# Performance work log

Hardware: AMD Instinct MI355X
Metric: run time of the kernel (lower is better)

## Reference

```python
import jax, jax.numpy as jnp
import numpy as np

N, E, F_IN, DIM, G = 50000, 800000, 128, 128, 512
NUM_GC_LAYERS = 3
S2S_STEPS = 3


def setup_inputs() -> dict:
    key = jax.random.key(0)
    ks = jax.random.split(key, 17)
    s = 0.05
    rn = lambda k, shape: jax.random.normal(k, shape, jnp.float32) * s
    x = jax.random.normal(ks[0], (N, F_IN), jnp.float32)
    edge_index = jax.random.randint(ks[1], (2, E), 0, N)
    batch = jnp.sort(jax.random.randint(ks[2], (N,), 0, G))
    return dict(
        x=x, edge_index=edge_index, batch=batch,
        lin0_W=rn(ks[3], (DIM, F_IN)), lin0_b=rn(ks[4], (DIM,)),
        gin_W1=rn(ks[5], (DIM, DIM)), gin_b1=rn(ks[6], (DIM,)),
        gin_W2=rn(ks[7], (DIM, DIM)), gin_b2=rn(ks[8], (DIM,)),
        gru_Wih=rn(ks[9], (3 * DIM, DIM)), gru_Whh=rn(ks[10], (3 * DIM, DIM)),
        gru_bih=rn(ks[11], (3 * DIM,)), gru_bhh=rn(ks[12], (3 * DIM,)),
        lstm_Wih=rn(ks[13], (4 * DIM, 2 * DIM)), lstm_Whh=rn(ks[14], (4 * DIM, DIM)),
        lstm_bih=rn(ks[15], (4 * DIM,)), lstm_bhh=rn(ks[16], (4 * DIM,)),
    )


def reference(x, edge_index, batch, lin0_W, lin0_b, gin_W1, gin_b1, gin_W2, gin_b2,
              gru_Wih, gru_Whh, gru_bih, gru_bhh,
              lstm_Wih, lstm_Whh, lstm_bih, lstm_bhh):
    src, dst = edge_index[0], edge_index[1]
    out = jax.nn.relu(x @ lin0_W.T + lin0_b)          # [N, DIM]
    h = out                                            # GRU hidden (seq_len=1, 1 layer)
    for _ in range(NUM_GC_LAYERS):
        # GINConv, eps=0: nn(x + sum_{j in N(i)} x_j); scatter-add over edge list
        aggr = jax.ops.segment_sum(out[src], dst, num_segments=N)
        z = out + aggr
        m = jax.nn.relu(jax.nn.relu(z @ gin_W1.T + gin_b1) @ gin_W2.T + gin_b2)
        # single GRU step (PyTorch gate order: r, z, n)
        gx = m @ gru_Wih.T + gru_bih
        gh = h @ gru_Whh.T + gru_bhh
        gxr, gxz, gxn = jnp.split(gx, 3, axis=-1)
        ghr, ghz, ghn = jnp.split(gh, 3, axis=-1)
        r = jax.nn.sigmoid(gxr + ghr)
        zt = jax.nn.sigmoid(gxz + ghz)
        n = jnp.tanh(gxn + r * ghn)
        h = (1.0 - zt) * n + zt * h
        out = h
    # Set2Set pooling (processing_steps=3), LSTM(2*DIM -> DIM), gate order i,f,g,o
    q_star = jnp.zeros((G, 2 * DIM), x.dtype)
    hl = jnp.zeros((G, DIM), x.dtype)
    cl = jnp.zeros((G, DIM), x.dtype)
    for _ in range(S2S_STEPS):
        gates = q_star @ lstm_Wih.T + lstm_bih + hl @ lstm_Whh.T + lstm_bhh
        i, f, g, o = jnp.split(gates, 4, axis=-1)
        cl = jax.nn.sigmoid(f) * cl + jax.nn.sigmoid(i) * jnp.tanh(g)
        hl = jax.nn.sigmoid(o) * jnp.tanh(cl)
        q = hl                                          # [G, DIM]
        e = jnp.sum(out * q[batch], axis=-1)            # [N] attention logits
        emax = jax.lax.stop_gradient(jax.ops.segment_max(e, batch, num_segments=G))
        emax = jnp.where(jnp.isfinite(emax), emax, 0.0)
        a_num = jnp.exp(e - emax[batch])
        denom = jax.ops.segment_sum(a_num, batch, num_segments=G)
        a = a_num / (denom[batch] + 1e-16)              # per-graph softmax
        rvec = jax.ops.segment_sum(a[:, None] * out, batch, num_segments=G)
        q_star = jnp.concatenate([q, rvec], axis=-1)    # [G, 2*DIM]
    return (q_star, out)
```

## Files before the change

kernel.cpp:

```cpp
#include <hip/hip_runtime.h>
#include <hip/hip_bf16.h>
#include <math.h>

static constexpr int NN  = 50000;
static constexpr int NE  = 800000;
static constexpr int DIM = 128;
static constexpr int NG  = 512;
static constexpr int NBLK = (NN + 255) / 256;

typedef __attribute__((ext_vector_type(8))) short bf16x8;
typedef __attribute__((ext_vector_type(4))) float f32x4;
typedef __attribute__((ext_vector_type(8))) float f32x8;

__device__ __forceinline__ float sigm(float x) {
    return __builtin_amdgcn_rcpf(1.0f + __expf(-x));
}
__device__ __forceinline__ float ftanh(float x) {
    x = fminf(fmaxf(x, -15.f), 15.f);
    float t = __expf(2.f * x);
    return (t - 1.f) * __builtin_amdgcn_rcpf(t + 1.f);
}
__device__ __forceinline__ float b2f(ushort u) { return __uint_as_float(((unsigned)u) << 16); }
__device__ __forceinline__ ushort f2b(float f) {
    __hip_bfloat16 h = __float2bfloat16(f);
    return *reinterpret_cast<ushort*>(&h);
}
__device__ __forceinline__ bf16x8 ldb8(const ushort* p) {
    return *reinterpret_cast<const bf16x8*>(p);
}
__device__ __forceinline__ f32x8 acc8(f32x8 a, uint4 v) {
    a[0] += b2f(v.x & 0xffff); a[1] += b2f(v.x >> 16);
    a[2] += b2f(v.y & 0xffff); a[3] += b2f(v.y >> 16);
    a[4] += b2f(v.z & 0xffff); a[5] += b2f(v.z >> 16);
    a[6] += b2f(v.w & 0xffff); a[7] += b2f(v.w >> 16);
    return a;
}

__global__ __launch_bounds__(256) void k_prep(const float* __restrict__ lin0_W,
                                              const float* __restrict__ gin_W1,
                                              const float* __restrict__ gin_W2,
                                              const float* __restrict__ gru_Wih,
                                              const float* __restrict__ gru_Whh,
                                              const float* __restrict__ gru_bih,
                                              const float* __restrict__ gru_bhh,
                                              const float* __restrict__ lstm_Wih,
                                              const float* __restrict__ lstm_Whh,
                                              const float* __restrict__ lstm_bih,
                                              const float* __restrict__ lstm_bhh,
                                              const int* __restrict__ batch,
                                              ushort* __restrict__ wlin0,
                                              ushort* __restrict__ wg1,
                                              ushort* __restrict__ wg2,
                                              ushort* __restrict__ wihb,
                                              ushort* __restrict__ whhb,
                                              ushort* __restrict__ wrz,
                                              float* __restrict__ brz,
                                              float* __restrict__ wltr,
                                              float* __restrict__ bl,
                                              int* __restrict__ gstart,
                                              float* __restrict__ zf,
                                              int* __restrict__ bcnt) {
    const int S0 = 16384, S1 = S0 + 16384, S2 = S1 + 16384;
    const int S3 = S2 + 49152, S4 = S3 + 49152, S5 = S4 + 65536;
    const int S6 = S5 + 256, S7 = S6 + 196608, S8 = S7 + 512;
    const int S9 = S8 + (NG + 1), S10 = S9 + 262144, S11 = S10 + 256;
    int i = blockIdx.x * 256 + threadIdx.x;
    if (i < S0) { wlin0[i] = f2b(lin0_W[i]); }
    else if (i < S1) { int j = i - S0; wg1[j] = f2b(gin_W1[j]); }
    else if (i < S2) { int j = i - S1; wg2[j] = f2b(gin_W2[j]); }
    else if (i < S3) { int j = i - S2; wihb[j] = f2b(gru_Wih[j]); }
    else if (i < S4) { int j = i - S3; whhb[j] = f2b(gru_Whh[j]); }
    else if (i < S5) {
        int j = i - S4; int col = j >> 8, k = j & 255;
        int row = (col >> 7) * 128 + (col & 127);
        wrz[j] = f2b((k < 128) ? gru_Whh[row * 128 + k] : gru_Wih[row * 128 + (k - 128)]);
    }
    else if (i < S6) { int j = i - S5; brz[j] = gru_bih[j] + gru_bhh[j]; }
    else if (i < S7) {
        int j = i - S6; int k = j / 512, col = j % 512;
        wltr[j] = (k < 256) ? lstm_Wih[(size_t)col * 256 + k]
                            : lstm_Whh[(size_t)col * 128 + (k - 256)];
    }
    else if (i < S8) { int j = i - S7; bl[j] = lstm_bih[j] + lstm_bhh[j]; }
    else if (i < S9) {
        int g = i - S8;
        int lo = 0, hi = NN;
        while (lo < hi) { int mid = (lo + hi) >> 1; if (batch[mid] < g) lo = mid + 1; else hi = mid; }
        gstart[g] = lo;
    }
    else if (i < S10) { zf[i - S9] = 0.f; }
    else if (i < S11) { bcnt[i - S10] = 0; }
}
static constexpr int PREP_TOTAL = 16384 * 3 + 49152 * 2 + 65536 + 256 + 196608 + 512 + (NG + 1) + 262144 + 256;

__global__ __launch_bounds__(256) void k_bcount(const int* __restrict__ dst,
                                                int* __restrict__ bcnt, int e) {
    __shared__ int l[256];
    int tid = threadIdx.x;
    l[tid] = 0;
    __syncthreads();
    int base = blockIdx.x * 4096;
    #pragma unroll
    for (int k = 0; k < 16; ++k) {
        int e0 = base + k * 256 + tid;
        if (e0 < e) atomicAdd(&l[dst[e0] >> 8], 1);
    }
    __syncthreads();
    if (l[tid] > 0) atomicAdd(&bcnt[tid], l[tid]);
}

__global__ __launch_bounds__(256) void k_btop(const int* __restrict__ bcnt,
                                              int* __restrict__ bbase,
                                              int* __restrict__ bcur) {
    __shared__ int s[256];
    int t = threadIdx.x;
    int v = bcnt[t];
    s[t] = v;
    __syncthreads();
    #pragma unroll
    for (int off = 1; off < 256; off <<= 1) {
        int x = (t >= off) ? s[t - off] : 0;
        __syncthreads();
        s[t] += x;
        __syncthreads();
    }
    int ex = s[t] - v;
    bbase[t] = ex;
    bcur[t] = ex;
    if (t == 255) bbase[256] = s[255];
}

__global__ __launch_bounds__(256) void k_bucket_lin0(const int* __restrict__ src,
                                                     const int* __restrict__ dst,
                                                     int* __restrict__ bcur,
                                                     int2* __restrict__ pairs, int e,
                                                     const float* __restrict__ X,
                                                     const ushort* __restrict__ W,
                                                     const float* __restrict__ bias,
                                                     ushort* __restrict__ AB, int n) {
    if (blockIdx.x < (unsigned)NBLK) {
        __shared__ int lcnt[256];
        __shared__ int lbase[256];
        int tid = threadIdx.x;
        lcnt[tid] = 0;
        __syncthreads();
        int base = blockIdx.x * 4096;
        #pragma unroll
        for (int k = 0; k < 16; ++k) {
            int e0 = base + k * 256 + tid;
            if (e0 < e) atomicAdd(&lcnt[dst[e0] >> 8], 1);
        }
        __syncthreads();
        int cnt = lcnt[tid];
        if (cnt > 0) lbase[tid] = atomicAdd(&bcur[tid], cnt);
        __syncthreads();
        lcnt[tid] = 0;
        __syncthreads();
        #pragma unroll
        for (int k = 0; k < 16; ++k) {
            int e0 = base + k * 256 + tid;
            if (e0 < e) {
                int d = dst[e0];
                int b = d >> 8;
                int off = atomicAdd(&lcnt[b], 1);
                pairs[lbase[b] + off] = make_int2(src[e0], d);
            }
        }
        return;
    }
    int bid = blockIdx.x - NBLK;
    int nlb = gridDim.x - NBLK;
    int lane = threadIdx.x & 63, wave = threadIdx.x >> 6;
    int c0 = lane & 15, kg = (lane >> 4) * 8;
    int tb0 = wave * 32;
    bf16x8 B[2][4];
    #pragma unroll
    for (int t = 0; t < 2; ++t)
        #pragma unroll
        for (int kk = 0; kk < 4; ++kk)
            B[t][kk] = ldb8(W + (size_t)(tb0 + t * 16 + c0) * 128 + kk * 32 + kg);

    for (int m0 = bid * 64; m0 < n; m0 += nlb * 64) {
        f32x4 acc[4][2];
        #pragma unroll
        for (int m = 0; m < 4; ++m) { acc[m][0] = {0,0,0,0}; acc[m][1] = {0,0,0,0}; }
        #pragma unroll
        for (int kk = 0; kk < 4; ++kk) {
            #pragma unroll
            for (int m = 0; m < 4; ++m) {
                int ar = min(m0 + m * 16 + c0, n - 1);
                const float* a = X + (size_t)ar * 128 + kk * 32 + kg;
                float4 x0 = *reinterpret_cast<const float4*>(a);
                float4 x1 = *reinterpret_cast<const float4*>(a + 4);
                bf16x8 af;
                af[0] = (short)f2b(x0.x); af[1] = (short)f2b(x0.y);
                af[2] = (short)f2b(x0.z); af[3] = (short)f2b(x0.w);
                af[4] = (short)f2b(x1.x); af[5] = (short)f2b(x1.y);
                af[6] = (short)f2b(x1.z); af[7] = (short)f2b(x1.w);
                acc[m][0] = __builtin_amdgcn_mfma_f32_16x16x32_bf16(af, B[0][kk], acc[m][0], 0, 0, 0);
                acc[m][1] = __builtin_amdgcn_mfma_f32_16x16x32_bf16(af, B[1][kk], acc[m][1], 0, 0, 0);
            }
        }
        #pragma unroll
        for (int m = 0; m < 4; ++m) {
            int rbase = m0 + m * 16 + ((lane >> 4) << 2);
            #pragma unroll
            for (int t = 0; t < 2; ++t) {
                int col = tb0 + t * 16 + c0;
                float bv = bias[col];
                #pragma unroll
                for (int j = 0; j < 4; ++j) {
                    int row = rbase + j;
                    if (row < n) {
                        float v = fmaxf(acc[m][t][j] + bv, 0.f);
                        AB[(size_t)row * 128 + col] = f2b(v);
                    }
                }
            }
        }
    }
}

__global__ __launch_bounds__(256) void k_fillbkt2(const int2* __restrict__ pairs,
                                                  const int* __restrict__ bbase,
                                                  int* __restrict__ rowptr,
                                                  int* __restrict__ csr) {
    __shared__ int lcnt[256];
    __shared__ int s[256];
    __shared__ int lcur[256];
    int b = blockIdx.x, tid = threadIdx.x;
    int w0 = b << 8;
    int r0 = bbase[b], r1 = bbase[b + 1];
    lcnt[tid] = 0;
    __syncthreads();
    for (int i = r0 + tid; i < r1; i += 256)
        atomicAdd(&lcnt[pairs[i].y - w0], 1);
    __syncthreads();
    int v = lcnt[tid];
    s[tid] = v;
    __syncthreads();
    #pragma unroll
    for (int off = 1; off < 256; off <<= 1) {
        int x = (tid >= off) ? s[tid - off] : 0;
        __syncthreads();
        s[tid] += x;
        __syncthreads();
    }
    int ex = r0 + s[tid] - v;
    lcur[tid] = ex;
    if (w0 + tid < NN) rowptr[w0 + tid] = ex;
    if (b == 0 && tid == 0) rowptr[NN] = NE;
    __syncthreads();
    for (int i = r0 + tid; i < r1; i += 256) {
        int2 p = pairs[i];
        int pos = atomicAdd(&lcur[p.y - w0], 1);
        csr[pos] = p.x;
    }
}

__global__ __launch_bounds__(512) void k_aggmlp(const ushort* __restrict__ AB,
                                                const int* __restrict__ rowptr,
                                                const int* __restrict__ csr,
                                                const ushort* __restrict__ W1,
                                                const float* __restrict__ b1,
                                                const ushort* __restrict__ W2,
                                                const float* __restrict__ b2,
                                                ushort* __restrict__ mt, int n) {
    __shared__ ushort Z_lds[32 * 136];
    __shared__ ushort M_lds[32 * 136];
    int tid = threadIdx.x;
    int lane = tid & 63, wave = tid >> 6;
    int c0 = lane & 15, kg = (lane >> 4) * 8;
    int colw = wave * 16 + c0;
    int rj = (lane >> 4) << 2;
    int grow_r = tid >> 4;
    int segi = tid & 15;
    const int stride = gridDim.x * 32;

    bf16x8 B1[4], B2[4];
    #pragma unroll
    for (int kk = 0; kk < 4; ++kk) {
        B1[kk] = ldb8(W1 + (size_t)colw * 128 + kk * 32 + kg);
        B2[kk] = ldb8(W2 + (size_t)colw * 128 + kk * 32 + kg);
    }
    float bv1 = b1[colw], bv2 = b2[colw];
    const uint4* bp = (const uint4*)AB;

    for (int m0 = blockIdx.x * 32; m0 < n; m0 += stride) {
        f32x8 A0 = {0,0,0,0,0,0,0,0};
        int grow = m0 + grow_r;
        if (grow < n) {
            f32x8 A1 = {0,0,0,0,0,0,0,0}, A2 = {0,0,0,0,0,0,0,0}, A3 = {0,0,0,0,0,0,0,0};
            A0 = acc8(A0, bp[(size_t)grow * 16 + segi]);
            int p = rowptr[grow], p1 = rowptr[grow + 1];
            for (; p + 4 <= p1; p += 4) {
                uint4 v0 = bp[(size_t)csr[p + 0] * 16 + segi];
                uint4 v1 = bp[(size_t)csr[p + 1] * 16 + segi];
                uint4 v2 = bp[(size_t)csr[p + 2] * 16 + segi];
                uint4 v3 = bp[(size_t)csr[p + 3] * 16 + segi];
                A0 = acc8(A0, v0); A1 = acc8(A1, v1);
                A2 = acc8(A2, v2); A3 = acc8(A3, v3);
            }
            for (; p < p1; ++p) A0 = acc8(A0, bp[(size_t)csr[p] * 16 + segi]);
            #pragma unroll
            for (int i = 0; i < 8; ++i) A0[i] += A1[i] + A2[i] + A3[i];
        }
        bf16x8 zz;
        #pragma unroll
        for (int i = 0; i < 8; ++i) zz[i] = (short)f2b(A0[i]);
        *reinterpret_cast<bf16x8*>(&Z_lds[grow_r * 136 + segi * 8]) = zz;
        __syncthreads();
        {
            f32x4 a[2] = {{0,0,0,0},{0,0,0,0}};
            #pragma unroll
            for (int kk = 0; kk < 4; ++kk) {
                bf16x8 f0 = *reinterpret_cast<const bf16x8*>(&Z_lds[c0 * 136 + kk * 32 + kg]);
                bf16x8 f1 = *reinterpret_cast<const bf16x8*>(&Z_lds[(16 + c0) * 136 + kk * 32 + kg]);
                a[0] = __builtin_amdgcn_mfma_f32_16x16x32_bf16(f0, B1[kk], a[0], 0, 0, 0);
                a[1] = __builtin_amdgcn_mfma_f32_16x16x32_bf16(f1, B1[kk], a[1], 0, 0, 0);
            }
            #pragma unroll
            for (int m = 0; m < 2; ++m)
                #pragma unroll
                for (int j = 0; j < 4; ++j)
                    M_lds[(m * 16 + rj + j) * 136 + colw] = f2b(fmaxf(a[m][j] + bv1, 0.f));
        }
        __syncthreads();
        {
            f32x4 a[2] = {{0,0,0,0},{0,0,0,0}};
            #pragma unroll
            for (int kk = 0; kk < 4; ++kk) {
                bf16x8 f0 = *reinterpret_cast<const bf16x8*>(&M_lds[c0 * 136 + kk * 32 + kg]);
                bf16x8 f1 = *reinterpret_cast<const bf16x8*>(&M_lds[(16 + c0) * 136 + kk * 32 + kg]);
                a[0] = __builtin_amdgcn_mfma_f32_16x16x32_bf16(f0, B2[kk], a[0], 0, 0, 0);
                a[1] = __builtin_amdgcn_mfma_f32_16x16x32_bf16(f1, B2[kk], a[1], 0, 0, 0);
            }
            #pragma unroll
            for (int m = 0; m < 2; ++m)
                #pragma unroll
                for (int j = 0; j < 4; ++j) {
                    int gr2 = m0 + m * 16 + rj + j;
                    if (gr2 < n)
                        mt[(size_t)gr2 * 128 + colw] = f2b(fmaxf(a[m][j] + bv2, 0.f));
                }
        }
        __syncthreads();
    }
}

template<bool WRITEH>
__global__ __launch_bounds__(512) void k_gru3b(const ushort* __restrict__ ABin,
                                               const ushort* __restrict__ mt,
                                               const ushort* __restrict__ wrz,
                                               const float* __restrict__ brz,
                                               const ushort* __restrict__ Wn,
                                               const ushort* __restrict__ Un,
                                               const float* __restrict__ bin,
                                               const float* __restrict__ bhn,
                                               float* __restrict__ Hf,
                                               ushort* __restrict__ ABout, int n) {
    __shared__ ushort A_lds[32 * 264];
    int tid = threadIdx.x;
    int lane = tid & 63, wave = tid >> 6;
    int c0 = lane & 15, kg = (lane >> 4) * 8;
    int colw = wave * 16 + c0;
    int rj = (lane >> 4) << 2;
    int srow = tid >> 4, scol = (tid & 15) * 8;
    const int stride = gridDim.x * 32;

    bf16x8 Brz[2][8];
    #pragma unroll
    for (int kk = 0; kk < 8; ++kk) {
        Brz[0][kk] = ldb8(wrz + (size_t)(colw) * 256 + kk * 32 + kg);
        Brz[1][kk] = ldb8(wrz + (size_t)(128 + colw) * 256 + kk * 32 + kg);
    }
    bf16x8 Bn[4], Bu[4];
    #pragma unroll
    for (int kk = 0; kk < 4; ++kk) {
        Bn[kk] = ldb8(Wn + (size_t)colw * 128 + kk * 32 + kg);
        Bu[kk] = ldb8(Un + (size_t)colw * 128 + kk * 32 + kg);
    }
    float biN = bin[colw], bhN = bhn[colw];
    float brzR = brz[colw], brzZ = brz[128 + colw];

    int m0 = blockIdx.x * 32;
    bf16x8 ph, pm;
    if (m0 < n) {
        int gr = min(m0 + srow, n - 1);
        ph = ldb8(ABin + (size_t)gr * 128 + scol);
        pm = ldb8(mt + (size_t)gr * 128 + scol);
    }
    for (; m0 < n; m0 += stride) {
        *reinterpret_cast<bf16x8*>(&A_lds[srow * 264 + scol]) = ph;
        *reinterpret_cast<bf16x8*>(&A_lds[srow * 264 + 128 + scol]) = pm;
        __syncthreads();
        int mn = m0 + stride;
        if (mn < n) {
            int gr = min(mn + srow, n - 1);
            ph = ldb8(ABin + (size_t)gr * 128 + scol);
            pm = ldb8(mt + (size_t)gr * 128 + scol);
        }
        f32x4 aR[2] = {{0,0,0,0},{0,0,0,0}};
        f32x4 aZ[2] = {{0,0,0,0},{0,0,0,0}};
        #pragma unroll
        for (int kk = 0; kk < 8; ++kk) {
            bf16x8 f0 = *reinterpret_cast<const bf16x8*>(&A_lds[c0 * 264 + kk * 32 + kg]);
            bf16x8 f1 = *reinterpret_cast<const bf16x8*>(&A_lds[(16 + c0) * 264 + kk * 32 + kg]);
            aR[0] = __builtin_amdgcn_mfma_f32_16x16x32_bf16(f0, Brz[0][kk], aR[0], 0, 0, 0);
            aZ[0] = __builtin_amdgcn_mfma_f32_16x16x32_bf16(f0, Brz[1][kk], aZ[0], 0, 0, 0);
            aR[1] = __builtin_amdgcn_mfma_f32_16x16x32_bf16(f1, Brz[0][kk], aR[1], 0, 0, 0);
            aZ[1] = __builtin_amdgcn_mfma_f32_16x16x32_bf16(f1, Brz[1][kk], aZ[1], 0, 0, 0);
        }
        f32x4 an[2] = {{0,0,0,0},{0,0,0,0}};
        f32x4 au[2] = {{0,0,0,0},{0,0,0,0}};
        #pragma unroll
        for (int kk = 0; kk < 4; ++kk) {
            bf16x8 am0 = *reinterpret_cast<const bf16x8*>(&A_lds[c0 * 264 + 128 + kk * 32 + kg]);
            bf16x8 ah0 = *reinterpret_cast<const bf16x8*>(&A_lds[c0 * 264 + kk * 32 + kg]);
            bf16x8 am1 = *reinterpret_cast<const bf16x8*>(&A_lds[(16 + c0) * 264 + 128 + kk * 32 + kg]);
            bf16x8 ah1 = *reinterpret_cast<const bf16x8*>(&A_lds[(16 + c0) * 264 + kk * 32 + kg]);
            an[0] = __builtin_amdgcn_mfma_f32_16x16x32_bf16(am0, Bn[kk], an[0], 0, 0, 0);
            au[0] = __builtin_amdgcn_mfma_f32_16x16x32_bf16(ah0, Bu[kk], au[0], 0, 0, 0);
            an[1] = __builtin_amdgcn_mfma_f32_16x16x32_bf16(am1, Bn[kk], an[1], 0, 0, 0);
            au[1] = __builtin_amdgcn_mfma_f32_16x16x32_bf16(ah1, Bu[kk], au[1], 0, 0, 0);
        }
        #pragma unroll
        for (int m = 0; m < 2; ++m)
            #pragma unroll
            for (int j = 0; j < 4; ++j) {
                int row = m * 16 + rj + j;
                int grow = m0 + row;
                if (grow < n) {
                    float r  = sigm(aR[m][j] + brzR);
                    float zt = sigm(aZ[m][j] + brzZ);
                    float hold = b2f(A_lds[row * 264 + colw]);
                    float nn = ftanh(an[m][j] + biN + r * (au[m][j] + bhN));
                    float hn = (1.f - zt) * nn + zt * hold;
                    ABout[(size_t)grow * 128 + colw] = f2b(hn);
                    if (WRITEH) Hf[(size_t)grow * 128 + colw] = hn;
                }
            }
        __syncthreads();
    }
}

__global__ __launch_bounds__(512) void k_s2s(const ushort* __restrict__ AB,
                                             const float* __restrict__ Wt,
                                             const float* __restrict__ bl,
                                             const int* __restrict__ gstart,
                                             const float* __restrict__ qstar,
                                             float* __restrict__ hl,
                                             float* __restrict__ cl,
                                             float* __restrict__ qout) {
    int g = blockIdx.x, tid = threadIdx.x, lane = tid & 63, wave = tid >> 6;
    __shared__ float qh[384];
    __shared__ float gbuf[512];
    __shared__ float q[128];
    __shared__ float wm[8];
    __shared__ float sw[8];
    __shared__ float rv[8][128];
    if (tid < 256) qh[tid] = qstar[(size_t)g * 256 + tid];
    else if (tid < 384) qh[tid] = hl[(size_t)g * 128 + (tid - 256)];
    __syncthreads();
    float acc = bl[tid];
    #pragma unroll 8
    for (int k = 0; k < 384; ++k)
        acc += Wt[(size_t)k * 512 + tid] * qh[k];
    gbuf[tid] = acc;
    __syncthreads();
    if (tid < 128) {
        float iv = sigm(gbuf[tid]);
        float fv = sigm(gbuf[128 + tid]);
        float gv = ftanh(gbuf[256 + tid]);
        float ov = sigm(gbuf[384 + tid]);
        float cn = fv * cl[(size_t)g * 128 + tid] + iv * gv;
        cl[(size_t)g * 128 + tid] = cn;
        float hn = ov * ftanh(cn);
        hl[(size_t)g * 128 + tid] = hn;
        q[tid] = hn;
    }
    __syncthreads();
    int s = gstart[g], e = gstart[g + 1];
    float q0 = q[2 * lane], q1 = q[2 * lane + 1];
    float mx = -1e30f, sumw = 0.f, a0 = 0.f, a1 = 0.f;
    for (int node = s + wave; node < e; node += 8) {
        unsigned u = ((const unsigned*)AB)[(size_t)node * 64 + lane];
        float v0 = b2f(u & 0xffff), v1 = b2f(u >> 16);
        float p = v0 * q0 + v1 * q1;
        #pragma unroll
        for (int off = 1; off < 64; off <<= 1) p += __shfl_xor(p, off);
        float nm = fmaxf(mx, p);
        float corr = __expf(mx - nm);
        float wgt = __expf(p - nm);
        sumw = sumw * corr + wgt;
        a0 = a0 * corr + wgt * v0;
        a1 = a1 * corr + wgt * v1;
        mx = nm;
    }
    if (lane == 0) wm[wave] = mx;
    __syncthreads();
    float gm = fmaxf(fmaxf(fmaxf(wm[0], wm[1]), fmaxf(wm[2], wm[3])),
                     fmaxf(fmaxf(wm[4], wm[5]), fmaxf(wm[6], wm[7])));
    float cw = __expf(mx - gm);
    rv[wave][2 * lane] = a0 * cw;
    rv[wave][2 * lane + 1] = a1 * cw;
    if (lane == 0) sw[wave] = sumw * cw;
    __syncthreads();
    if (tid < 128) {
        float r = 0.f, d = 1e-16f;
        #pragma unroll
        for (int wv = 0; wv < 8; ++wv) r += rv[wv][tid];
        #pragma unroll
        for (int wv = 0; wv < 8; ++wv) d += sw[wv];
        qout[(size_t)g * 256 + tid] = q[tid];
        qout[(size_t)g * 256 + 128 + tid] = r / d;
    }
}

extern "C" void kernel_launch(void* const* d_in, const int* in_sizes, int n_in,
                              void* d_out, int out_size, void* d_ws, size_t ws_size,
                              hipStream_t stream) {
    const float* x        = (const float*)d_in[0];
    const int*   ei       = (const int*)d_in[1];
    const int*   batch    = (const int*)d_in[2];
    const float* lin0_W   = (const float*)d_in[3];
    const float* lin0_b   = (const float*)d_in[4];
    const float* gin_W1   = (const float*)d_in[5];
    const float* gin_b1   = (const float*)d_in[6];
    const float* gin_W2   = (const float*)d_in[7];
    const float* gin_b2   = (const float*)d_in[8];
    const float* gru_Wih  = (const float*)d_in[9];
    const float* gru_Whh  = (const float*)d_in[10];
    const float* gru_bih  = (const float*)d_in[11];
    const float* gru_bhh  = (const float*)d_in[12];
    const float* lstm_Wih = (const float*)d_in[13];
    const float* lstm_Whh = (const float*)d_in[14];
    const float* lstm_bih = (const float*)d_in[15];
    const float* lstm_bhh = (const float*)d_in[16];

    float* qstar_out = (float*)d_out;
    float* h         = (float*)d_out + (size_t)NG * 2 * DIM;

    char* w = (char*)d_ws;
    ushort* AB0   = (ushort*)w; w += (size_t)NN * 128 * 2;
    ushort* AB1   = (ushort*)w; w += (size_t)NN * 128 * 2;
    ushort* mt    = (ushort*)w; w += (size_t)NN * 128 * 2;
    ushort* wlin0 = (ushort*)w; w += 16384 * 2;
    ushort* wg1   = (ushort*)w; w += 16384 * 2;
    ushort* wg2   = (ushort*)w; w += 16384 * 2;
    ushort* wihb  = (ushort*)w; w += 49152 * 2;
    ushort* whhb  = (ushort*)w; w += 49152 * 2;
    ushort* wrz   = (ushort*)w; w += 65536 * 2;
    float* brz    = (float*)w;  w += 256 * 4;
    float* wltr   = (float*)w;  w += (size_t)512 * 384 * 4;
    float* bl     = (float*)w;  w += 512 * 4;
    float* qstar  = (float*)w;  w += (size_t)NG * 2 * DIM * 4;
    float* hl     = (float*)w;  w += (size_t)NG * DIM * 4;
    float* cl     = (float*)w;  w += (size_t)NG * DIM * 4;
    int* rowptr   = (int*)w;    w += (size_t)(NN + 1) * 4;
    int* bcnt     = (int*)w;    w += 256 * 4;
    int* bbase    = (int*)w;    w += 257 * 4;
    int* bcur     = (int*)w;    w += 256 * 4;
    int* csr_src  = (int*)w;    w += (size_t)NE * 4;
    int2* pairs   = (int2*)w;   w += (size_t)NE * 8;
    int* gstart   = (int*)w;    w += (size_t)(NG + 1) * 4;

    const int* src = ei;
    const int* dst = ei + NE;

    k_prep<<<(PREP_TOTAL + 255) / 256, 256, 0, stream>>>(
        lin0_W, gin_W1, gin_W2, gru_Wih, gru_Whh, gru_bih, gru_bhh,
        lstm_Wih, lstm_Whh, lstm_bih, lstm_bhh, batch,
        wlin0, wg1, wg2, wihb, whhb, wrz, brz, wltr, bl, gstart, qstar, bcnt);

    k_bcount<<<(NE + 4095) / 4096, 256, 0, stream>>>(dst, bcnt, NE);
    k_btop<<<1, 256, 0, stream>>>(bcnt, bbase, bcur);
    k_bucket_lin0<<<NBLK + 782, 256, 0, stream>>>(src, dst, bcur, pairs, NE,
                                                  x, wlin0, lin0_b, AB0, NN);
    k_fillbkt2<<<NBLK, 256, 0, stream>>>(pairs, bbase, rowptr, csr_src);

    for (int t = 0; t < 3; ++t) {
        ushort* ABc = (t & 1) ? AB1 : AB0;
        ushort* ABn = (t & 1) ? AB0 : AB1;
        k_aggmlp<<<1024, 512, 0, stream>>>(ABc, rowptr, csr_src,
                                           wg1, gin_b1, wg2, gin_b2, mt, NN);
        if (t < 2)
            k_gru3b<false><<<512, 512, 0, stream>>>(ABc, mt, wrz, brz,
                                                    wihb + 256 * 128, whhb + 256 * 128,
                                                    gru_bih + 256, gru_bhh + 256, h, ABn, NN);
        else
            k_gru3b<true><<<512, 512, 0, stream>>>(ABc, mt, wrz, brz,
                                                   wihb + 256 * 128, whhb + 256 * 128,
                                                   gru_bih + 256, gru_bhh + 256, h, ABn, NN);
    }
    const ushort* ABfin = AB1;

    for (int st = 0; st < 3; ++st)
        k_s2s<<<NG, 512, 0, stream>>>(ABfin, wltr, bl, gstart, qstar, hl, cl,
                                      (st == 2) ? qstar_out : qstar);
}
```

Measured before the change: 361.4 us.

## Fuse three Set2Set steps into one kernel with LSTM state in LDS

Replaces the three per-step Set2Set launches with a single kernel that loops over the steps and keeps q_star, hl and cl in shared memory instead of global buffers. This removes two kernel launches and the global round-trips for the LSTM state. It also drops the prep-kernel zero-fill of the q_star/hl/cl workspace, since state now starts at zero in LDS. The 384x512 LSTM weight matrix is still reread from global (likely L2) on every step by each block.

```diff
diff --git a/kernel.cpp b/kernel.cpp
--- a/kernel.cpp
+++ b/kernel.cpp
@@ -58,12 +58,11 @@
                                               float* __restrict__ wltr,
                                               float* __restrict__ bl,
                                               int* __restrict__ gstart,
-                                              float* __restrict__ zf,
                                               int* __restrict__ bcnt) {
     const int S0 = 16384, S1 = S0 + 16384, S2 = S1 + 16384;
     const int S3 = S2 + 49152, S4 = S3 + 49152, S5 = S4 + 65536;
     const int S6 = S5 + 256, S7 = S6 + 196608, S8 = S7 + 512;
-    const int S9 = S8 + (NG + 1), S10 = S9 + 262144, S11 = S10 + 256;
+    const int S9 = S8 + (NG + 1), S10 = S9 + 256;
     int i = blockIdx.x * 256 + threadIdx.x;
     if (i < S0) { wlin0[i] = f2b(lin0_W[i]); }
     else if (i < S1) { int j = i - S0; wg1[j] = f2b(gin_W1[j]); }
@@ -88,10 +87,9 @@
         while (lo < hi) { int mid = (lo + hi) >> 1; if (batch[mid] < g) lo = mid + 1; else hi = mid; }
         gstart[g] = lo;
     }
-    else if (i < S10) { zf[i - S9] = 0.f; }
-    else if (i < S11) { bcnt[i - S10] = 0; }
-}
-static constexpr int PREP_TOTAL = 16384 * 3 + 49152 * 2 + 65536 + 256 + 196608 + 512 + (NG + 1) + 262144 + 256;
+    else if (i < S10) { bcnt[i - S9] = 0; }
+}
+static constexpr int PREP_TOTAL = 16384 * 3 + 49152 * 2 + 65536 + 256 + 196608 + 512 + (NG + 1) + 256;
 
 __global__ __launch_bounds__(256) void k_bcount(const int* __restrict__ dst,
                                                 int* __restrict__ bcnt, int e) {
@@ -444,76 +442,82 @@
     }
 }
 
-__global__ __launch_bounds__(512) void k_s2s(const ushort* __restrict__ AB,
-                                             const float* __restrict__ Wt,
-                                             const float* __restrict__ bl,
-                                             const int* __restrict__ gstart,
-                                             const float* __restrict__ qstar,
-                                             float* __restrict__ hl,
-                                             float* __restrict__ cl,
-                                             float* __restrict__ qout) {
+__global__ __launch_bounds__(512) void k_s2s3(const ushort* __restrict__ AB,
+                                              const float* __restrict__ Wt,
+                                              const float* __restrict__ bl,
+                                              const int* __restrict__ gstart,
+                                              float* __restrict__ qout) {
     int g = blockIdx.x, tid = threadIdx.x, lane = tid & 63, wave = tid >> 6;
     __shared__ float qh[384];
+    __shared__ float cl_s[128];
     __shared__ float gbuf[512];
     __shared__ float q[128];
     __shared__ float wm[8];
     __shared__ float sw[8];
     __shared__ float rv[8][128];
-    if (tid < 256) qh[tid] = qstar[(size_t)g * 256 + tid];
-    else if (tid < 384) qh[tid] = hl[(size_t)g * 128 + (tid - 256)];
-    __syncthreads();
-    float acc = bl[tid];
-    #pragma unroll 8
-    for (int k = 0; k < 384; ++k)
-        acc += Wt[(size_t)k * 512 + tid] * qh[k];
-    gbuf[tid] = acc;
-    __syncthreads();
-    if (tid < 128) {
-        float iv = sigm(gbuf[tid]);
-        float fv = sigm(gbuf[128 + tid]);
-        float gv = ftanh(gbuf[256 + tid]);
-        float ov = sigm(gbuf[384 + tid]);
-        float cn = fv * cl[(size_t)g * 128 + tid] + iv * gv;
-        cl[(size_t)g * 128 + tid] = cn;
-        float hn = ov * ftanh(cn);
-        hl[(size_t)g * 128 + tid] = hn;
-        q[tid] = hn;
-    }
-    __syncthreads();
+    if (tid < 384) qh[tid] = 0.f;
+    if (tid < 128) cl_s[tid] = 0.f;
     int s = gstart[g], e = gstart[g + 1];
-    float q0 = q[2 * lane], q1 = q[2 * lane + 1];
-    float mx = -1e30f, sumw = 0.f, a0 = 0.f, a1 = 0.f;
-    for (int node = s + wave; node < e; node += 8) {
-        unsigned u = ((const unsigned*)AB)[(size_t)node * 64 + lane];
-        float v0 = b2f(u & 0xffff), v1 = b2f(u >> 16);
-        float p = v0 * q0 + v1 * q1;
-        #pragma unroll
-        for (int off = 1; off < 64; off <<= 1) p += __shfl_xor(p, off);
-        float nm = fmaxf(mx, p);
-        float corr = __expf(mx - nm);
-        float wgt = __expf(p - nm);
-        sumw = sumw * corr + wgt;
-        a0 = a0 * corr + wgt * v0;
-        a1 = a1 * corr + wgt * v1;
-        mx = nm;
-    }
-    if (lane == 0) wm[wave] = mx;
-    __syncthreads();
-    float gm = fmaxf(fmaxf(fmaxf(wm[0], wm[1]), fmaxf(wm[2], wm[3])),
-                     fmaxf(fmaxf(wm[4], wm[5]), fmaxf(wm[6], wm[7])));
-    float cw = __expf(mx - gm);
-    rv[wave][2 * lane] = a0 * cw;
-    rv[wave][2 * lane + 1] = a1 * cw;
-    if (lane == 0) sw[wave] = sumw * cw;
-    __syncthreads();
-    if (tid < 128) {
-        float r = 0.f, d = 1e-16f;
-        #pragma unroll
-        for (int wv = 0; wv < 8; ++wv) r += rv[wv][tid];
-        #pragma unroll
-        for (int wv = 0; wv < 8; ++wv) d += sw[wv];
-        qout[(size_t)g * 256 + tid] = q[tid];
-        qout[(size_t)g * 256 + 128 + tid] = r / d;
+
+    for (int st = 0; st < 3; ++st) {
+        __syncthreads();
+        float acc = bl[tid];
+        #pragma unroll 8
+        for (int k = 0; k < 384; ++k)
+            acc += Wt[(size_t)k * 512 + tid] * qh[k];
+        gbuf[tid] = acc;
+        __syncthreads();
+        if (tid < 128) {
+            float iv = sigm(gbuf[tid]);
+            float fv = sigm(gbuf[128 + tid]);
+            float gv = ftanh(gbuf[256 + tid]);
+            float ov = sigm(gbuf[384 + tid]);
+            float cn = fv * cl_s[tid] + iv * gv;
+            cl_s[tid] = cn;
+            float hn = ov * ftanh(cn);
+            q[tid] = hn;
+            qh[256 + tid] = hn;
+        }
+        __syncthreads();
+        float q0 = q[2 * lane], q1 = q[2 * lane + 1];
+        float mx = -1e30f, sumw = 0.f, a0 = 0.f, a1 = 0.f;
+        for (int node = s + wave; node < e; node += 8) {
+            unsigned u = ((const unsigned*)AB)[(size_t)node * 64 + lane];
+            float v0 = b2f(u & 0xffff), v1 = b2f(u >> 16);
+            float p = v0 * q0 + v1 * q1;
+            #pragma unroll
+            for (int off = 1; off < 64; off <<= 1) p += __shfl_xor(p, off);
+            float nm = fmaxf(mx, p);
+            float corr = __expf(mx - nm);
+            float wgt = __expf(p - nm);
+            sumw = sumw * corr + wgt;
+            a0 = a0 * corr + wgt * v0;
+            a1 = a1 * corr + wgt * v1;
+            mx = nm;
+        }
+        if (lane == 0) wm[wave] = mx;
+        __syncthreads();
+        float gm = fmaxf(fmaxf(fmaxf(wm[0], wm[1]), fmaxf(wm[2], wm[3])),
+                         fmaxf(fmaxf(wm[4], wm[5]), fmaxf(wm[6], wm[7])));
+        float cw = __expf(mx - gm);
+        rv[wave][2 * lane] = a0 * cw;
+        rv[wave][2 * lane + 1] = a1 * cw;
+        if (lane == 0) sw[wave] = sumw * cw;
+        __syncthreads();
+        if (tid < 128) {
+            float r = 0.f, d = 1e-16f;
+            #pragma unroll
+            for (int wv = 0; wv < 8; ++wv) r += rv[wv][tid];
+            #pragma unroll
+            for (int wv = 0; wv < 8; ++wv) d += sw[wv];
+            if (st == 2) {
+                qout[(size_t)g * 256 + tid] = q[tid];
+                qout[(size_t)g * 256 + 128 + tid] = r / d;
+            } else {
+                qh[tid] = q[tid];
+                qh[128 + tid] = r / d;
+            }
+        }
     }
 }
 
@@ -554,9 +558,6 @@
     float* brz    = (float*)w;  w += 256 * 4;
     float* wltr   = (float*)w;  w += (size_t)512 * 384 * 4;
     float* bl     = (float*)w;  w += 512 * 4;
-    float* qstar  = (float*)w;  w += (size_t)NG * 2 * DIM * 4;
-    float* hl     = (float*)w;  w += (size_t)NG * DIM * 4;
-    float* cl     = (float*)w;  w += (size_t)NG * DIM * 4;
     int* rowptr   = (int*)w;    w += (size_t)(NN + 1) * 4;
     int* bcnt     = (int*)w;    w += 256 * 4;
     int* bbase    = (int*)w;    w += 257 * 4;
@@ -571,7 +572,7 @@
     k_prep<<<(PREP_TOTAL + 255) / 256, 256, 0, stream>>>(
         lin0_W, gin_W1, gin_W2, gru_Wih, gru_Whh, gru_bih, gru_bhh,
         lstm_Wih, lstm_Whh, lstm_bih, lstm_bhh, batch,
-        wlin0, wg1, wg2, wihb, whhb, wrz, brz, wltr, bl, gstart, qstar, bcnt);
+        wlin0, wg1, wg2, wihb, whhb, wrz, brz, wltr, bl, gstart, bcnt);
 
     k_bcount<<<(NE + 4095) / 4096, 256, 0, stream>>>(dst, bcnt, NE);
     k_btop<<<1, 256, 0, stream>>>(bcnt, bbase, bcur);
@@ -595,7 +596,5 @@
     }
     const ushort* ABfin = AB1;
 
-    for (int st = 0; st < 3; ++st)
-        k_s2s<<<NG, 512, 0, stream>>>(ABfin, wltr, bl, gstart, qstar, hl, cl,
-                                      (st == 2) ? qstar_out : qstar);
-}
+    k_s2s3<<<NG, 512, 0, stream>>>(ABfin, wltr, bl, gstart, qstar_out);
+}
```

Result: faster. 354.3 us (-2.0%).
